# Optimization experiments

Hardware: AMD Instinct MI355X
Metric: run time of the kernel (lower is better)

The kernel has to match this reference:

```python
import jax, jax.numpy as jnp
import numpy as np

N, TO, TI, H = 8, 2048, 2048, 128
MASK_FILL = -99999.0  # module uses -99999.0, not -inf


def setup_inputs() -> dict:
    key = jax.random.key(0)
    kq, kv, km = jax.random.split(key, 3)
    queries = jax.random.normal(kq, (N, TO, H), dtype=jnp.float32)
    values = jax.random.normal(kv, (N, TI, H), dtype=jnp.float32)
    # mask is applied to scores.view(-1, Ti) -> shape (N*To, Ti), True = masked
    mask = jax.random.randint(km, (N * TO, TI), 0, 2).astype(bool)
    return {"queries": queries, "values": values, "mask": mask}


def reference(queries, values, mask):
    n, to, h = queries.shape
    ti = values.shape[1]
    # N x To x Ti scores (no 1/sqrt(H) scaling in the original)
    scores = jnp.einsum("nth,nsh->nts", queries, values)
    scores = jnp.where(mask.reshape(n, to, ti), MASK_FILL, scores)
    attention_distribution = jax.nn.softmax(scores, axis=-1)
    attention_output = jnp.einsum("nts,nsh->nth", attention_distribution, values)
    return attention_output, attention_distribution
```

## Files before the change

kernel.cpp:

```cpp
#include <hip/hip_runtime.h>

#define NB  8
#define TOQ 2048
#define TIV 2048
#define HD  128

typedef float f32x4 __attribute__((ext_vector_type(4)));
typedef short s16x8 __attribute__((ext_vector_type(8)));
typedef unsigned short ushort8v __attribute__((ext_vector_type(8)));

__device__ __forceinline__ unsigned short f2bf(float f) {
    unsigned u = __float_as_uint(f);
    return (unsigned short)((u + 0x7FFFu + ((u >> 16) & 1u)) >> 16);
}
__device__ __forceinline__ float bf2f(unsigned short h) {
    return __uint_as_float(((unsigned)h) << 16);
}

__device__ __forceinline__ void split8(const float4 a, const float4 b,
                                       ushort8v& h, ushort8v& l) {
    const float x[8] = {a.x, a.y, a.z, a.w, b.x, b.y, b.z, b.w};
    #pragma unroll
    for (int j = 0; j < 8; ++j) {
        const unsigned short hi = f2bf(x[j]);
        h[j] = hi;
        l[j] = f2bf(x[j] - bf2f(hi));
    }
}

__device__ __forceinline__ void gload16(const void* g, void* l) {
    __builtin_amdgcn_global_load_lds(
        (const __attribute__((address_space(1))) void*)g,
        (__attribute__((address_space(3))) void*)l, 16, 0, 0);
}

__global__ __launch_bounds__(256) void k0_split(
    const float* __restrict__ Q, const float* __restrict__ V,
    unsigned short* __restrict__ Qh, unsigned short* __restrict__ Ql,
    unsigned short* __restrict__ Vh, unsigned short* __restrict__ Vl)
{
    const size_t i = ((size_t)blockIdx.x * 256 + threadIdx.x) * 8;
    const float* src = blockIdx.y ? V : Q;
    unsigned short* dh = blockIdx.y ? Vh : Qh;
    unsigned short* dl = blockIdx.y ? Vl : Ql;
    const float4 a = *(const float4*)&src[i];
    const float4 b = *(const float4*)&src[i + 4];
    ushort8v h, l;
    split8(a, b, h, l);
    *(ushort8v*)&dh[i] = h;
    *(ushort8v*)&dl[i] = l;
}

__global__ __launch_bounds__(256) void k0_vt(
    const float* __restrict__ V, unsigned short* __restrict__ VTf)
{
    __shared__ unsigned short tile[64][68];
    const int n  = blockIdx.z;
    const int s0 = blockIdx.x * 64;
    const int h0 = blockIdx.y * 64;
    const int t  = threadIdx.x;

    #pragma unroll
    for (int it = 0; it < 4; ++it) {
        const int f = t + it * 256;
        const int r = f >> 4;
        const int c = f & 15;
        const float4 v = *(const float4*)&V[((size_t)(n * TIV + s0 + r)) * HD + h0 + 4 * c];
        tile[4 * c + 0][r] = f2bf(v.x);
        tile[4 * c + 1][r] = f2bf(v.y);
        tile[4 * c + 2][r] = f2bf(v.z);
        tile[4 * c + 3][r] = f2bf(v.w);
    }
    __syncthreads();

    #pragma unroll
    for (int it = 0; it < 2; ++it) {
        const int s    = t * 2 + it;
        const int k32i = s >> 8;
        const int fni  = (s >> 6) & 3;
        const int l    = s & 63;
        const int hh   = fni * 16 + (l & 15);
        const int kloc = k32i * 32 + ((l >> 4) * 8);
        ushort8v o;
        #pragma unroll
        for (int j = 0; j < 8; ++j) o[j] = tile[hh][kloc + j];
        const size_t k32g = (size_t)(s0 >> 5) + k32i;
        const size_t fng  = (size_t)(h0 >> 4) + fni;
        *(ushort8v*)&VTf[(((size_t)n * 64 + k32g) * 8 + fng) * 512 + (size_t)l * 8] = o;
    }
}

__global__ __launch_bounds__(256) void k1_lds(
    const unsigned short* __restrict__ QhG, const unsigned short* __restrict__ QlG,
    const unsigned short* __restrict__ VhG, const unsigned short* __restrict__ VlG,
    const int* __restrict__ M, float* __restrict__ E,
    float* __restrict__ part)
{
    __shared__ unsigned short qh_l[128 * 32], ql_l[128 * 32];
    __shared__ unsigned short vh_l[128 * 32], vl_l[128 * 32];

    const int n    = blockIdx.z;
    const int tt   = blockIdx.y * 128;
    const int ts   = blockIdx.x * 128;
    const int t    = threadIdx.x;
    const int lane = t & 63;
    const int wave = t >> 6;
    const int wr   = wave >> 1;
    const int wc   = wave & 1;
    const int lr   = lane & 15;
    const int kg   = lane >> 4;

    f32x4 acc[4][4];
    #pragma unroll
    for (int i = 0; i < 4; ++i)
        #pragma unroll
        for (int j = 0; j < 4; ++j) acc[i][j] = (f32x4)0.f;

    for (int h0 = 0; h0 < HD; h0 += 32) {
        #pragma unroll
        for (int j = 0; j < 2; ++j) {
            const int c    = wave * 128 + j * 64 + lane;
            const int row  = c >> 2;
            const int kb   = (c & 3) * 8;
            const int lb   = (wave * 128 + j * 64) * 8;
            const size_t qo = ((size_t)(n * TOQ + tt + row)) * HD + h0 + kb;
            const size_t vo = ((size_t)(n * TIV + ts + row)) * HD + h0 + kb;
            gload16(QhG + qo, qh_l + lb);
            gload16(QlG + qo, ql_l + lb);
            gload16(VhG + vo, vh_l + lb);
            gload16(VlG + vo, vl_l + lb);
        }
        __syncthreads();

        s16x8 aH[4], aL[4];
        #pragma unroll
        for (int fm = 0; fm < 4; ++fm) {
            const int off = (wr * 64 + fm * 16 + lr) * 32 + kg * 8;
            aH[fm] = *(const s16x8*)(vh_l + off);
            aL[fm] = *(const s16x8*)(vl_l + off);
        }
        #pragma unroll
        for (int fn = 0; fn < 4; ++fn) {
            const int off = (wc * 64 + fn * 16 + lr) * 32 + kg * 8;
            const s16x8 bH = *(const s16x8*)(qh_l + off);
            const s16x8 bL = *(const s16x8*)(ql_l + off);
            #pragma unroll
            for (int fm = 0; fm < 4; ++fm) {
                acc[fm][fn] = __builtin_amdgcn_mfma_f32_16x16x32_bf16(aH[fm], bH, acc[fm][fn], 0, 0, 0);
                acc[fm][fn] = __builtin_amdgcn_mfma_f32_16x16x32_bf16(aH[fm], bL, acc[fm][fn], 0, 0, 0);
                acc[fm][fn] = __builtin_amdgcn_mfma_f32_16x16x32_bf16(aL[fm], bH, acc[fm][fn], 0, 0, 0);
            }
        }
        __syncthreads();
    }

    #pragma unroll
    for (int fn = 0; fn < 4; ++fn) {
        const int to_g = tt + wc * 64 + fn * 16 + lr;
        const size_t rowbase = ((size_t)n * TOQ + to_g) * TIV;
        float rs = 0.f;
        #pragma unroll
        for (int fm = 0; fm < 4; ++fm) {
            const int ti_g = ts + wr * 64 + fm * 16 + kg * 4;
            const int4 mv = *(const int4*)&M[rowbase + ti_g];
            float4 e;
            e.x = mv.x ? 0.f : __expf(acc[fm][fn][0]);
            e.y = mv.y ? 0.f : __expf(acc[fm][fn][1]);
            e.z = mv.z ? 0.f : __expf(acc[fm][fn][2]);
            e.w = mv.w ? 0.f : __expf(acc[fm][fn][3]);
            *(float4*)&E[rowbase + ti_g] = e;
            rs += (e.x + e.y) + (e.z + e.w);
        }
        rs += __shfl_xor(rs, 16, 64);
        rs += __shfl_xor(rs, 32, 64);
        if (kg == 0)
            part[((size_t)n * TOQ + to_g) * 32 + blockIdx.x * 2 + wr] = rs;
    }
}

__global__ __launch_bounds__(256) void k1_reg(
    const float* __restrict__ Q, const float* __restrict__ V,
    const int* __restrict__ M, float* __restrict__ E,
    float* __restrict__ part)
{
    __shared__ unsigned short qhi[128 * 32], qlo[128 * 32];
    __shared__ unsigned short vhi[128 * 32], vlo[128 * 32];

    const int n    = blockIdx.z;
    const int tt   = blockIdx.y * 128;
    const int ts   = blockIdx.x * 128;
    const int t    = threadIdx.x;
    const int lane = t & 63;
    const int wave = t >> 6;
    const int wr   = wave >> 1;
    const int wc   = wave & 1;
    const int lr   = lane & 15;
    const int kg   = lane >> 4;

    const float* Qb = Q + ((size_t)n * TOQ + tt) * HD;
    const float* Vb = V + ((size_t)n * TIV + ts) * HD;

    f32x4 acc[4][4];
    #pragma unroll
    for (int i = 0; i < 4; ++i)
        #pragma unroll
        for (int j = 0; j < 4; ++j) acc[i][j] = (f32x4)0.f;

    for (int h0 = 0; h0 < HD; h0 += 32) {
        #pragma unroll
        for (int it = 0; it < 2; ++it) {
            const int i   = t + it * 256;
            const int row = i >> 2;
            const int kb  = i & 3;
            const float* qs = Qb + (size_t)row * HD + h0 + kb * 8;
            const float* vs = Vb + (size_t)row * HD + h0 + kb * 8;
            const float4 q0 = *(const float4*)qs, q1 = *(const float4*)(qs + 4);
            const float4 v0 = *(const float4*)vs, v1 = *(const float4*)(vs + 4);
            ushort8v qh, ql, vh, vl;
            split8(q0, q1, qh, ql);
            split8(v0, v1, vh, vl);
            *(ushort8v*)(qhi + i * 8) = qh;
            *(ushort8v*)(qlo + i * 8) = ql;
            *(ushort8v*)(vhi + i * 8) = vh;
            *(ushort8v*)(vlo + i * 8) = vl;
        }
        __syncthreads();

        s16x8 aH[4], aL[4];
        #pragma unroll
        for (int fm = 0; fm < 4; ++fm) {
            const int off = (wr * 64 + fm * 16 + lr) * 32 + kg * 8;
            aH[fm] = *(const s16x8*)(vhi + off);
            aL[fm] = *(const s16x8*)(vlo + off);
        }
        #pragma unroll
        for (int fn = 0; fn < 4; ++fn) {
            const int off = (wc * 64 + fn * 16 + lr) * 32 + kg * 8;
            const s16x8 bH = *(const s16x8*)(qhi + off);
            const s16x8 bL = *(const s16x8*)(qlo + off);
            #pragma unroll
            for (int fm = 0; fm < 4; ++fm) {
                acc[fm][fn] = __builtin_amdgcn_mfma_f32_16x16x32_bf16(aH[fm], bH, acc[fm][fn], 0, 0, 0);
                acc[fm][fn] = __builtin_amdgcn_mfma_f32_16x16x32_bf16(aH[fm], bL, acc[fm][fn], 0, 0, 0);
                acc[fm][fn] = __builtin_amdgcn_mfma_f32_16x16x32_bf16(aL[fm], bH, acc[fm][fn], 0, 0, 0);
            }
        }
        __syncthreads();
    }

    #pragma unroll
    for (int fn = 0; fn < 4; ++fn) {
        const int to_g = tt + wc * 64 + fn * 16 + lr;
        const size_t rowbase = ((size_t)n * TOQ + to_g) * TIV;
        float rs = 0.f;
        #pragma unroll
        for (int fm = 0; fm < 4; ++fm) {
            const int ti_g = ts + wr * 64 + fm * 16 + kg * 4;
            const int4 mv = *(const int4*)&M[rowbase + ti_g];
            float4 e;
            e.x = mv.x ? 0.f : __expf(acc[fm][fn][0]);
            e.y = mv.y ? 0.f : __expf(acc[fm][fn][1]);
            e.z = mv.z ? 0.f : __expf(acc[fm][fn][2]);
            e.w = mv.w ? 0.f : __expf(acc[fm][fn][3]);
            *(float4*)&E[rowbase + ti_g] = e;
            rs += (e.x + e.y) + (e.z + e.w);
        }
        rs += __shfl_xor(rs, 16, 64);
        rs += __shfl_xor(rs, 32, 64);
        if (kg == 0)
            part[((size_t)n * TOQ + to_g) * 32 + blockIdx.x * 2 + wr] = rs;
    }
}

__global__ __launch_bounds__(256) void k2_rowsum(
    const float* __restrict__ part, float* __restrict__ rec)
{
    const int row = blockIdx.x * 256 + threadIdx.x;
    const float4* p4 = (const float4*)(part + (size_t)row * 32);
    float s = 0.f;
    #pragma unroll
    for (int i = 0; i < 8; ++i) {
        const float4 v = p4[i];
        s += (v.x + v.y) + (v.z + v.w);
    }
    rec[row] = 1.f / s;
}

__global__ __launch_bounds__(512) void k3_pv(
    float* __restrict__ EP, const unsigned short* __restrict__ VTf,
    const float* __restrict__ rec, float* __restrict__ O)
{
    __shared__ __attribute__((aligned(16))) char smem[50688];
    unsigned short* stg = (unsigned short*)smem;
    float*          red = (float*)smem;

    const int n    = blockIdx.y;
    const int r0   = blockIdx.x * 32;
    const int t    = threadIdx.x;
    const int wave = t >> 6;
    const int lane = t & 63;
    const int p    = wave >> 2;
    const int q    = wave & 3;
    const int lr   = lane & 15;
    const int kg   = lane >> 4;

    const size_t rowbase0 = (size_t)n * TOQ + r0 + p * 16;
    unsigned short* wstg = stg + wave * (16 * 136);

    float rv[4];
    #pragma unroll
    for (int r = 0; r < 4; ++r) rv[r] = rec[rowbase0 + 4 * r + kg];

    f32x4 acc[8];
    #pragma unroll
    for (int fn = 0; fn < 8; ++fn) acc[fn] = (f32x4)0.f;

    const unsigned short* VTn = VTf + (size_t)n * 64 * 8 * 512;

    for (int kb = 0; kb < 4; ++kb) {
        const int kwin = q * 512 + kb * 128;

        #pragma unroll
        for (int r = 0; r < 4; ++r) {
            const int row_l = 4 * r + kg;
            float* Erow = EP + (rowbase0 + row_l) * TIV + kwin + lr * 8;
            const float4 e0 = *(const float4*)Erow;
            const float4 e1 = *(const float4*)(Erow + 4);
            const float rc = rv[r];
            float4 p0, p1;
            p0.x = e0.x * rc; p0.y = e0.y * rc; p0.z = e0.z * rc; p0.w = e0.w * rc;
            p1.x = e1.x * rc; p1.y = e1.y * rc; p1.z = e1.z * rc; p1.w = e1.w * rc;
            *(float4*)Erow       = p0;
            *(float4*)(Erow + 4) = p1;
            ushort8v s8;
            s8[0] = f2bf(p0.x); s8[1] = f2bf(p0.y); s8[2] = f2bf(p0.z); s8[3] = f2bf(p0.w);
            s8[4] = f2bf(p1.x); s8[5] = f2bf(p1.y); s8[6] = f2bf(p1.z); s8[7] = f2bf(p1.w);
            *(ushort8v*)&wstg[row_l * 136 + lr * 8] = s8;
        }

        #pragma unroll
        for (int ks = 0; ks < 4; ++ks) {
            const s16x8 a = *(const s16x8*)&wstg[lr * 136 + ks * 32 + kg * 8];
            const int k32 = q * 16 + kb * 4 + ks;
            const unsigned short* bbase = VTn + ((size_t)k32 * 8) * 512 + (size_t)lane * 8;
            #pragma unroll
            for (int fn = 0; fn < 8; ++fn) {
                const s16x8 b = *(const s16x8*)(bbase + (size_t)fn * 512);
                acc[fn] = __builtin_amdgcn_mfma_f32_16x16x32_bf16(a, b, acc[fn], 0, 0, 0);
            }
        }
    }

    __syncthreads();
    if (q != 0) {
        #pragma unroll
        for (int fn = 0; fn < 8; ++fn)
            #pragma unroll
            for (int ri = 0; ri < 4; ++ri)
                red[(((size_t)p * 3 + (q - 1)) * 16 + kg * 4 + ri) * 132 + fn * 16 + lr] = acc[fn][ri];
    }
    __syncthreads();
    if (q == 0) {
        #pragma unroll
        for (int fn = 0; fn < 8; ++fn) {
            #pragma unroll
            for (int ri = 0; ri < 4; ++ri) {
                const int orow = r0 + p * 16 + kg * 4 + ri;
                float o = acc[fn][ri];
                o += red[(((size_t)p * 3 + 0) * 16 + kg * 4 + ri) * 132 + fn * 16 + lr];
                o += red[(((size_t)p * 3 + 1) * 16 + kg * 4 + ri) * 132 + fn * 16 + lr];
                o += red[(((size_t)p * 3 + 2) * 16 + kg * 4 + ri) * 132 + fn * 16 + lr];
                O[((size_t)n * TOQ + orow) * HD + fn * 16 + lr] = o;
            }
        }
    }
}

extern "C" void kernel_launch(void* const* d_in, const int* in_sizes, int n_in,
                              void* d_out, int out_size, void* d_ws, size_t ws_size,
                              hipStream_t stream)
{
    const float* Q = (const float*)d_in[0];
    const float* V = (const float*)d_in[1];
    const int*   M = (const int*)d_in[2];

    float* O = (float*)d_out;
    float* P = O + (size_t)NB * TOQ * HD;

    char* ws = (char*)d_ws;
    const size_t partB  = (size_t)NB * TOQ * 32 * 4;
    const size_t vtB    = (size_t)NB * 64 * 8 * 512 * 2;
    const size_t elems  = (size_t)NB * TOQ * HD;
    const size_t sbytes = elems * 2;

    float*          recb = (float*)ws;
    float*          part = (float*)(ws + (1 << 16));
    unsigned short* VTf  = (unsigned short*)(ws + (1 << 16) + partB);
    const size_t splitOff = (1 << 16) + partB + vtB;
    const size_t need1    = splitOff + 4 * sbytes;

    k0_vt<<<dim3(TIV / 64, HD / 64, NB), 256, 0, stream>>>(V, VTf);

    if (ws_size >= need1) {
        unsigned short* Qh = (unsigned short*)(ws + splitOff);
        unsigned short* Ql = (unsigned short*)(ws + splitOff + sbytes);
        unsigned short* Vh = (unsigned short*)(ws + splitOff + 2 * sbytes);
        unsigned short* Vl = (unsigned short*)(ws + splitOff + 3 * sbytes);
        k0_split<<<dim3((unsigned)(elems / 8 / 256), 2), 256, 0, stream>>>(Q, V, Qh, Ql, Vh, Vl);
        k1_lds  <<<dim3(TIV / 128, TOQ / 128, NB), 256, 0, stream>>>(Qh, Ql, Vh, Vl, M, P, part);
    } else {
        k1_reg  <<<dim3(TIV / 128, TOQ / 128, NB), 256, 0, stream>>>(Q, V, M, P, part);
    }

    k2_rowsum<<<dim3(NB * TOQ / 256), 256, 0, stream>>>(part, recb);
    k3_pv    <<<dim3(TOQ / 32, NB), 512, 0, stream>>>(P, VTf, recb, O);
}
```

Before: 183.0 us.

## Store unnormalized exp scores as bf16 and prefetch them in PV kernel

```diff
diff --git a/kernel.cpp b/kernel.cpp
--- a/kernel.cpp
+++ b/kernel.cpp
@@ -7,6 +7,7 @@
 
 typedef float f32x4 __attribute__((ext_vector_type(4)));
 typedef short s16x8 __attribute__((ext_vector_type(8)));
+typedef unsigned short ushort4v __attribute__((ext_vector_type(4)));
 typedef unsigned short ushort8v __attribute__((ext_vector_type(8)));
 
 __device__ __forceinline__ unsigned short f2bf(float f) {
@@ -51,7 +52,7 @@
     *(ushort8v*)&dl[i] = l;
 }
 
-__global__ __launch_bounds__(256) void k0_vt(
+__global__ __launch_bounds__(256) void k0_vtf(
     const float* __restrict__ V, unsigned short* __restrict__ VTf)
 {
     __shared__ unsigned short tile[64][68];
@@ -90,10 +91,44 @@
     }
 }
 
-__global__ __launch_bounds__(256) void k1_lds(
+__global__ __launch_bounds__(256) void k0_vt_old(
+    const float* __restrict__ V, unsigned short* __restrict__ VT)
+{
+    __shared__ unsigned short tile[64][68];
+    const int n  = blockIdx.z;
+    const int s0 = blockIdx.x * 64;
+    const int h0 = blockIdx.y * 64;
+    const int t  = threadIdx.x;
+
+    #pragma unroll
+    for (int it = 0; it < 4; ++it) {
+        const int f = t + it * 256;
+        const int r = f >> 4;
+        const int c = f & 15;
+        const float4 v = *(const float4*)&V[((size_t)(n * TIV + s0 + r)) * HD + h0 + 4 * c];
+        tile[4 * c + 0][r] = f2bf(v.x);
+        tile[4 * c + 1][r] = f2bf(v.y);
+        tile[4 * c + 2][r] = f2bf(v.z);
+        tile[4 * c + 3][r] = f2bf(v.w);
+    }
+    __syncthreads();
+
+    #pragma unroll
+    for (int it = 0; it < 2; ++it) {
+        const int f  = t + it * 256;
+        const int hh = f >> 3;
+        const int sc = f & 7;
+        ushort8v o;
+        #pragma unroll
+        for (int j = 0; j < 8; ++j) o[j] = tile[hh][8 * sc + j];
+        *(ushort8v*)&VT[((size_t)(n * HD + h0 + hh)) * TIV + s0 + 8 * sc] = o;
+    }
+}
+
+__global__ __launch_bounds__(512) void k1_w8(
     const unsigned short* __restrict__ QhG, const unsigned short* __restrict__ QlG,
     const unsigned short* __restrict__ VhG, const unsigned short* __restrict__ VlG,
-    const int* __restrict__ M, float* __restrict__ E,
+    const int* __restrict__ M, unsigned short* __restrict__ Eb,
     float* __restrict__ part)
 {
     __shared__ unsigned short qh_l[128 * 32], ql_l[128 * 32];
@@ -105,24 +140,23 @@
     const int t    = threadIdx.x;
     const int lane = t & 63;
     const int wave = t >> 6;
-    const int wr   = wave >> 1;
-    const int wc   = wave & 1;
+    const int wr   = wave >> 2;
+    const int wc   = wave & 3;
     const int lr   = lane & 15;
     const int kg   = lane >> 4;
 
-    f32x4 acc[4][4];
+    f32x4 acc[4][2];
     #pragma unroll
     for (int i = 0; i < 4; ++i)
         #pragma unroll
-        for (int j = 0; j < 4; ++j) acc[i][j] = (f32x4)0.f;
+        for (int j = 0; j < 2; ++j) acc[i][j] = (f32x4)0.f;
 
     for (int h0 = 0; h0 < HD; h0 += 32) {
-        #pragma unroll
-        for (int j = 0; j < 2; ++j) {
-            const int c    = wave * 128 + j * 64 + lane;
-            const int row  = c >> 2;
-            const int kb   = (c & 3) * 8;
-            const int lb   = (wave * 128 + j * 64) * 8;
+        {
+            const int c   = wave * 64 + lane;
+            const int row = c >> 2;
+            const int kb  = (c & 3) * 8;
+            const int lb  = wave * 512;
             const size_t qo = ((size_t)(n * TOQ + tt + row)) * HD + h0 + kb;
             const size_t vo = ((size_t)(n * TIV + ts + row)) * HD + h0 + kb;
             gload16(QhG + qo, qh_l + lb);
@@ -140,8 +174,8 @@
             aL[fm] = *(const s16x8*)(vl_l + off);
         }
         #pragma unroll
-        for (int fn = 0; fn < 4; ++fn) {
-            const int off = (wc * 64 + fn * 16 + lr) * 32 + kg * 8;
+        for (int fn = 0; fn < 2; ++fn) {
+            const int off = (wc * 32 + fn * 16 + lr) * 32 + kg * 8;
             const s16x8 bH = *(const s16x8*)(qh_l + off);
             const s16x8 bL = *(const s16x8*)(ql_l + off);
             #pragma unroll
@@ -155,8 +189,8 @@
     }
 
     #pragma unroll
-    for (int fn = 0; fn < 4; ++fn) {
-        const int to_g = tt + wc * 64 + fn * 16 + lr;
+    for (int fn = 0; fn < 2; ++fn) {
+        const int to_g = tt + wc * 32 + fn * 16 + lr;
         const size_t rowbase = ((size_t)n * TOQ + to_g) * TIV;
         float rs = 0.f;
         #pragma unroll
@@ -168,7 +202,10 @@
             e.y = mv.y ? 0.f : __expf(acc[fm][fn][1]);
             e.z = mv.z ? 0.f : __expf(acc[fm][fn][2]);
             e.w = mv.w ? 0.f : __expf(acc[fm][fn][3]);
-            *(float4*)&E[rowbase + ti_g] = e;
+            ushort4v eb;
+            eb[0] = f2bf(e.x); eb[1] = f2bf(e.y);
+            eb[2] = f2bf(e.z); eb[3] = f2bf(e.w);
+            *(ushort4v*)&Eb[rowbase + ti_g] = eb;
             rs += (e.x + e.y) + (e.z + e.w);
         }
         rs += __shfl_xor(rs, 16, 64);
@@ -286,9 +323,9 @@
     rec[row] = 1.f / s;
 }
 
-__global__ __launch_bounds__(512) void k3_pv(
-    float* __restrict__ EP, const unsigned short* __restrict__ VTf,
-    const float* __restrict__ rec, float* __restrict__ O)
+__global__ __launch_bounds__(512) void k3_pf(
+    const unsigned short* __restrict__ Eb, const unsigned short* __restrict__ VTf,
+    const float* __restrict__ rec, float* __restrict__ P, float* __restrict__ O)
 {
     __shared__ __attribute__((aligned(16))) char smem[50688];
     unsigned short* stg = (unsigned short*)smem;
@@ -317,25 +354,36 @@
 
     const unsigned short* VTn = VTf + (size_t)n * 64 * 8 * 512;
 
+    ushort8v ev[4];
+    #pragma unroll
+    for (int r = 0; r < 4; ++r)
+        ev[r] = *(const ushort8v*)&Eb[(rowbase0 + 4 * r + kg) * TIV + q * 512 + lr * 8];
+
     for (int kb = 0; kb < 4; ++kb) {
         const int kwin = q * 512 + kb * 128;
 
         #pragma unroll
         for (int r = 0; r < 4; ++r) {
             const int row_l = 4 * r + kg;
-            float* Erow = EP + (rowbase0 + row_l) * TIV + kwin + lr * 8;
-            const float4 e0 = *(const float4*)Erow;
-            const float4 e1 = *(const float4*)(Erow + 4);
-            const float rc = rv[r];
+            float pv[8];
+            #pragma unroll
+            for (int j = 0; j < 8; ++j) pv[j] = bf2f(ev[r][j]) * rv[r];
             float4 p0, p1;
-            p0.x = e0.x * rc; p0.y = e0.y * rc; p0.z = e0.z * rc; p0.w = e0.w * rc;
-            p1.x = e1.x * rc; p1.y = e1.y * rc; p1.z = e1.z * rc; p1.w = e1.w * rc;
-            *(float4*)Erow       = p0;
-            *(float4*)(Erow + 4) = p1;
+            p0.x = pv[0]; p0.y = pv[1]; p0.z = pv[2]; p0.w = pv[3];
+            p1.x = pv[4]; p1.y = pv[5]; p1.z = pv[6]; p1.w = pv[7];
+            float* Prow = P + (rowbase0 + row_l) * TIV + kwin + lr * 8;
+            *(float4*)Prow       = p0;
+            *(float4*)(Prow + 4) = p1;
             ushort8v s8;
-            s8[0] = f2bf(p0.x); s8[1] = f2bf(p0.y); s8[2] = f2bf(p0.z); s8[3] = f2bf(p0.w);
-            s8[4] = f2bf(p1.x); s8[5] = f2bf(p1.y); s8[6] = f2bf(p1.z); s8[7] = f2bf(p1.w);
+            #pragma unroll
+            for (int j = 0; j < 8; ++j) s8[j] = f2bf(pv[j]);
             *(ushort8v*)&wstg[row_l * 136 + lr * 8] = s8;
+        }
+
+        if (kb < 3) {
+            #pragma unroll
+            for (int r = 0; r < 4; ++r)
+                ev[r] = *(const ushort8v*)&Eb[(rowbase0 + 4 * r + kg) * TIV + kwin + 128 + lr * 8];
         }
 
         #pragma unroll
@@ -376,6 +424,81 @@
     }
 }
 
+__global__ __launch_bounds__(512) void k3_pv_old(
+    float* __restrict__ EP, const unsigned short* __restrict__ VT,
+    const float* __restrict__ rec, float* __restrict__ O)
+{
+    __shared__ float red[2][3][16][132];
+
+    const int n    = blockIdx.y;
+    const int r0   = blockIdx.x * 32;
+    const int t    = threadIdx.x;
+    const int wave = t >> 6;
+    const int lane = t & 63;
+    const int p    = wave >> 2;
+    const int q    = wave & 3;
+    const int lr   = lane & 15;
+    const int kg   = lane >> 4;
+
+    const int rowg = r0 + p * 16 + lr;
+    const float rc = rec[n * TOQ + rowg];
+    float* Erow = EP + ((size_t)n * TOQ + rowg) * TIV;
+    const unsigned short* VTb = VT + (size_t)n * HD * TIV;
+
+    f32x4 acc[8];
+    #pragma unroll
+    for (int fn = 0; fn < 8; ++fn) acc[fn] = (f32x4)0.f;
+
+    const int kbase = q * 512 + kg * 8;
+
+    #pragma unroll 2
+    for (int k0 = 0; k0 < 512; k0 += 32) {
+        const int k = kbase + k0;
+        const float4 e0 = *(const float4*)&Erow[k];
+        const float4 e1 = *(const float4*)&Erow[k + 4];
+        float4 p0, p1;
+        p0.x = e0.x * rc; p0.y = e0.y * rc; p0.z = e0.z * rc; p0.w = e0.w * rc;
+        p1.x = e1.x * rc; p1.y = e1.y * rc; p1.z = e1.z * rc; p1.w = e1.w * rc;
+        *(float4*)&Erow[k]     = p0;
+        *(float4*)&Erow[k + 4] = p1;
+
+        s16x8 a;
+        a[0] = (short)f2bf(p0.x); a[1] = (short)f2bf(p0.y);
+        a[2] = (short)f2bf(p0.z); a[3] = (short)f2bf(p0.w);
+        a[4] = (short)f2bf(p1.x); a[5] = (short)f2bf(p1.y);
+        a[6] = (short)f2bf(p1.z); a[7] = (short)f2bf(p1.w);
+
+        #pragma unroll
+        for (int fn = 0; fn < 8; ++fn) {
+            const s16x8 b = *(const s16x8*)&VTb[(size_t)(fn * 16 + lr) * TIV + k];
+            acc[fn] = __builtin_amdgcn_mfma_f32_16x16x32_bf16(a, b, acc[fn], 0, 0, 0);
+        }
+    }
+
+    if (q != 0) {
+        #pragma unroll
+        for (int fn = 0; fn < 8; ++fn)
+            #pragma unroll
+            for (int ri = 0; ri < 4; ++ri)
+                red[p][q - 1][kg * 4 + ri][fn * 16 + lr] = acc[fn][ri];
+    }
+    __syncthreads();
+    if (q == 0) {
+        #pragma unroll
+        for (int fn = 0; fn < 8; ++fn) {
+            #pragma unroll
+            for (int ri = 0; ri < 4; ++ri) {
+                const int orow = r0 + p * 16 + kg * 4 + ri;
+                float o = acc[fn][ri];
+                o += red[p][0][kg * 4 + ri][fn * 16 + lr];
+                o += red[p][1][kg * 4 + ri][fn * 16 + lr];
+                o += red[p][2][kg * 4 + ri][fn * 16 + lr];
+                O[((size_t)n * TOQ + orow) * HD + fn * 16 + lr] = o;
+            }
+        }
+    }
+}
+
 extern "C" void kernel_launch(void* const* d_in, const int* in_sizes, int n_in,
                               void* d_out, int out_size, void* d_ws, size_t ws_size,
                               hipStream_t stream)
@@ -392,26 +515,30 @@
     const size_t vtB    = (size_t)NB * 64 * 8 * 512 * 2;
     const size_t elems  = (size_t)NB * TOQ * HD;
     const size_t sbytes = elems * 2;
+    const size_t ebB    = (size_t)NB * TOQ * TIV * 2;
 
     float*          recb = (float*)ws;
     float*          part = (float*)(ws + (1 << 16));
-    unsigned short* VTf  = (unsigned short*)(ws + (1 << 16) + partB);
+    unsigned short* VT   = (unsigned short*)(ws + (1 << 16) + partB);
     const size_t splitOff = (1 << 16) + partB + vtB;
-    const size_t need1    = splitOff + 4 * sbytes;
-
-    k0_vt<<<dim3(TIV / 64, HD / 64, NB), 256, 0, stream>>>(V, VTf);
-
-    if (ws_size >= need1) {
+    const size_t ebOff    = splitOff + 4 * sbytes;
+    const size_t need2    = ebOff + ebB;
+
+    if (ws_size >= need2) {
         unsigned short* Qh = (unsigned short*)(ws + splitOff);
         unsigned short* Ql = (unsigned short*)(ws + splitOff + sbytes);
         unsigned short* Vh = (unsigned short*)(ws + splitOff + 2 * sbytes);
         unsigned short* Vl = (unsigned short*)(ws + splitOff + 3 * sbytes);
+        unsigned short* Eb = (unsigned short*)(ws + ebOff);
+        k0_vtf  <<<dim3(TIV / 64, HD / 64, NB), 256, 0, stream>>>(V, VT);
         k0_split<<<dim3((unsigned)(elems / 8 / 256), 2), 256, 0, stream>>>(Q, V, Qh, Ql, Vh, Vl);
-        k1_lds  <<<dim3(TIV / 128, TOQ / 128, NB), 256, 0, stream>>>(Qh, Ql, Vh, Vl, M, P, part);
+        k1_w8   <<<dim3(TIV / 128, TOQ / 128, NB), 512, 0, stream>>>(Qh, Ql, Vh, Vl, M, Eb, part);
+        k2_rowsum<<<dim3(NB * TOQ / 256), 256, 0, stream>>>(part, recb);
+        k3_pf   <<<dim3(TOQ / 32, NB), 512, 0, stream>>>(Eb, VT, recb, P, O);
     } else {
+        k0_vt_old<<<dim3(TIV / 64, HD / 64, NB), 256, 0, stream>>>(V, VT);
         k1_reg  <<<dim3(TIV / 128, TOQ / 128, NB), 256, 0, stream>>>(Q, V, M, P, part);
-    }
-
-    k2_rowsum<<<dim3(NB * TOQ / 256), 256, 0, stream>>>(part, recb);
-    k3_pv    <<<dim3(TOQ / 32, NB), 512, 0, stream>>>(P, VTf, recb, O);
-}
+        k2_rowsum<<<dim3(NB * TOQ / 256), 256, 0, stream>>>(part, recb);
+        k3_pv_old<<<dim3(TOQ / 32, NB), 512, 0, stream>>>(P, VT, recb, O);
+    }
+}
```

Measured after the change: 181.8 us. About the same (-0.7%).
